# Kernel tuning notes

Hardware: AMD Instinct MI355X
Metric: run time of the kernel (lower is better)

## Reference

```python
import jax, jax.numpy as jnp
import numpy as np


def setup_inputs() -> dict:
    key = jax.random.key(0)
    k1, k2, k3, k4 = jax.random.split(key, 4)
    B, N, D = 4, 2048, 1024
    scale = 1.0 / np.sqrt(D)
    return {
        "x": jax.random.normal(k1, (B, N, D), dtype=jnp.float32),
        "Wq": jax.random.normal(k2, (D, D), dtype=jnp.float32) * scale,
        "Wk": jax.random.normal(k3, (D, D), dtype=jnp.float32) * scale,
        "Wv": jax.random.normal(k4, (D, D), dtype=jnp.float32) * scale,
    }


def reference(x, Wq, Wk, Wv):
    # x: [b, n, d_in]; W*: [d_out, d_in] (torch Linear convention y = x @ W.T)
    q = jnp.einsum("bnd,od->bno", x, Wq)
    k = jnp.einsum("bnd,od->bno", x, Wk)
    v = jnp.einsum("bnd,od->bno", x, Wv)
    n = x.shape[1]
    d_out = k.shape[-1]
    scores = jnp.einsum("bqd,bkd->bqk", q, k)  # [b, n, n]
    causal = jnp.triu(jnp.ones((n, n), dtype=bool), k=1)  # True above diagonal
    scores = jnp.where(causal[None, :, :], -jnp.inf, scores)
    # NOTE: faithful to source -- softmax over dim=1 (query axis), not dim=-1
    attn = jax.nn.softmax(scores / jnp.sqrt(jnp.float32(d_out)), axis=1)
    # dropout p=0.0 (eval): identity
    return jnp.einsum("bqk,bkd->bqd", attn, v)
```

## Files before the change

### kernel.cpp

```cpp
#include <hip/hip_runtime.h>
#include <stdint.h>
#include <math.h>


typedef __attribute__((ext_vector_type(8))) short short8;
typedef __attribute__((ext_vector_type(4))) float f32x4;

static __device__ __forceinline__ ushort f2bf(float f) {
  union { float f; uint32_t u; } v; v.f = f;
  uint32_t r = v.u + 0x7FFFu + ((v.u >> 16) & 1u);
  return (ushort)(r >> 16);
}
static __device__ __forceinline__ float bf2f(ushort u) {
  union { uint32_t u; float f; } v; v.u = ((uint32_t)u) << 16;
  return v.f;
}

static __device__ __forceinline__ void gload_lds16(const ushort* g, ushort* l) {
  __builtin_amdgcn_global_load_lds(
      (const __attribute__((address_space(1))) void*)g,
      (__attribute__((address_space(3))) void*)l, 16, 0, 0);
}

#define SBAR()   __builtin_amdgcn_s_barrier()
#define SCHED0() __builtin_amdgcn_sched_barrier(0)
#define WAITL0() do { asm volatile("s_waitcnt lgkmcnt(0)" ::: "memory"); SCHED0(); } while (0)
#define WAITV4() asm volatile("s_waitcnt vmcnt(4)" ::: "memory")
#define WAITV3() asm volatile("s_waitcnt vmcnt(3)" ::: "memory")
#define WAITV0() asm volatile("s_waitcnt vmcnt(0)" ::: "memory")

__global__ void cast_all(const float* __restrict__ x, const float* __restrict__ Wq,
                         const float* __restrict__ Wk, const float* __restrict__ Wv,
                         ushort* __restrict__ xb, ushort* __restrict__ Wb,
                         int n_x4, int n_w4) {
  int i = blockIdx.x * blockDim.x + threadIdx.x;
  const float* src; ushort* dst; int off;
  if (i < n_x4) { src = x; dst = xb; off = i; }
  else {
    int j = i - n_x4;
    int z = j / n_w4;
    off = j - z * n_w4;
    src = (z == 0) ? Wq : (z == 1) ? Wk : Wv;
    dst = Wb + (long)z * n_w4 * 4;
  }
  float4 v = ((const float4*)src)[off];
  ushort4 o;
  o.x = f2bf(v.x); o.y = f2bf(v.y); o.z = f2bf(v.z); o.w = f2bf(v.w);
  ((ushort4*)dst)[off] = o;
}

__global__ __launch_bounds__(512, 4) void proj_all(
    const ushort* __restrict__ xb, const ushort* __restrict__ Wb,
    ushort* __restrict__ QK, ushort* __restrict__ Vt)
{
  const int D = 1024;
  const long BND = 8388608;
  int L = blockIdx.x;
  L = (L & 7) * 96 + (L >> 3);

  const ushort* Ab; const ushort* Bb;
  int bm0, bn0;
  if (L < 512) {
    int rem = L & 255;
    bm0 = (rem >> 3) * 256;
    bn0 = (rem & 7) * 128;
    Ab = xb;
    Bb = Wb + (long)(L >> 8) * D * D;
  } else {
    int rem = L - 512;
    bm0 = (rem >> 6) * 256;
    bn0 = (rem & 63) * 128;
    Ab = Wb + 2L * D * D;
    Bb = xb;
  }

  const int nk = 32;

  __shared__ uint4 lds_v[73728 / 16];
  char* lds = (char*)lds_v;

  const int tid  = threadIdx.x;
  const int lane = tid & 63;
  const int wave = tid >> 6;
  const int wr   = wave >> 1;
  const int wc   = wave & 1;
  const int fr   = lane & 15;
  const int fg   = lane >> 4;

  f32x4 acc[4][4];
#pragma unroll
  for (int i = 0; i < 4; ++i)
#pragma unroll
    for (int j = 0; j < 4; ++j) acc[i][j] = (f32x4){0.f, 0.f, 0.f, 0.f};

  auto STAGE = [&](int tt) {
    if (tt >= nk) return;
    char* slab = lds + (tt % 3) * 24576;
#pragma unroll
    for (int u = 0; u < 2; ++u) {
      int s = u * 512 + tid;
      int row = s >> 2;
      int cc = (s & 3) ^ ((row >> 1) & 3);
      gload_lds16(Ab + (long)(bm0 + row) * D + tt * 32 + cc * 8,
                  (ushort*)(slab + s * 16));
    }
    {
      int s = tid;
      int row = s >> 2;
      int cc = (s & 3) ^ ((row >> 1) & 3);
      gload_lds16(Bb + (long)(bn0 + row) * D + tt * 32 + cc * 8,
                  (ushort*)(slab + 16384 + s * 16));
    }
  };

  STAGE(0); STAGE(1);
  WAITV3();
  SBAR();

  for (int t = 0; t < nk; ++t) {
    char* slab = lds + (t % 3) * 24576;
    STAGE(t + 2);

    short8 a[4], b[4];
#pragma unroll
    for (int i = 0; i < 4; ++i) {
      int row = wr * 64 + i * 16 + fr;
      int cc = fg ^ ((row >> 1) & 3);
      a[i] = *(const short8*)(slab + row * 64 + cc * 16);
    }
#pragma unroll
    for (int j = 0; j < 4; ++j) {
      int row = wc * 64 + j * 16 + fr;
      int cc = fg ^ ((row >> 1) & 3);
      b[j] = *(const short8*)(slab + 16384 + row * 64 + cc * 16);
    }
    WAITL0();
    __builtin_amdgcn_s_setprio(1);
#pragma unroll
    for (int i = 0; i < 4; ++i)
#pragma unroll
      for (int j = 0; j < 4; ++j)
        acc[i][j] = __builtin_amdgcn_mfma_f32_16x16x32_bf16(a[i], b[j], acc[i][j], 0, 0, 0);
    __builtin_amdgcn_s_setprio(0);

    if (t + 2 < nk) { WAITV3(); } else { WAITV0(); }
    SBAR();
  }

  if (L < 512) {
    ushort* Cb = QK + (long)(L >> 8) * BND;
#pragma unroll
    for (int i = 0; i < 4; ++i)
#pragma unroll
      for (int j = 0; j < 4; ++j)
#pragma unroll
        for (int r = 0; r < 4; ++r) {
          int row = bm0 + wr * 64 + i * 16 + fg * 4 + r;
          int col = bn0 + wc * 64 + j * 16 + fr;
          Cb[(long)row * D + col] = f2bf(acc[i][j][r]);
        }
  } else {
    ushort* Cb = Vt + (long)(bn0 >> 11) * D * 2048;
#pragma unroll
    for (int i = 0; i < 4; ++i)
#pragma unroll
      for (int j = 0; j < 4; ++j)
#pragma unroll
        for (int r = 0; r < 4; ++r) {
          int row = bm0 + wr * 64 + i * 16 + fg * 4 + r;
          int col = (bn0 + wc * 64 + j * 16 + fr) & 2047;
          Cb[(long)row * 2048 + col] = f2bf(acc[i][j][r]);
        }
  }
}

__global__ __launch_bounds__(256, 3) void gemm_s(
    const ushort* __restrict__ Q, const ushort* __restrict__ Kb, ushort* __restrict__ S,
    float* __restrict__ pMg, float* __restrict__ pZg)
{
  const int NQ = 2048, D = 1024;
  int bid = blockIdx.x;
  bid = (bid & 7) * 68 + (bid >> 3);
  const int b = bid / 136;
  int t = bid - b * 136;
  int i = (int)((sqrtf(8.f * t + 1.f) - 1.f) * 0.5f);
  while ((i + 1) * (i + 2) / 2 <= t) ++i;
  while (i * (i + 1) / 2 > t) --i;
  const int j = t - i * (i + 1) / 2;
  const int bm0 = i * 128;
  const int bn0 = j * 128;

  const ushort* Ab = Q + (long)b * NQ * D;
  const ushort* Bb = Kb + (long)b * NQ * D;

  const int nk = 32;

  __shared__ uint4 lds_v[49152 / 16];
  char* lds = (char*)lds_v;

  const int tid  = threadIdx.x;
  const int lane = tid & 63;
  const int wave = tid >> 6;
  const int wr   = wave >> 1;
  const int wc   = wave & 1;
  const int fr   = lane & 15;
  const int fg   = lane >> 4;

  f32x4 acc[4][4];
#pragma unroll
  for (int ii = 0; ii < 4; ++ii)
#pragma unroll
    for (int jj = 0; jj < 4; ++jj) acc[ii][jj] = (f32x4){0.f, 0.f, 0.f, 0.f};

  auto STAGE = [&](int tt) {
    if (tt >= nk) return;
    char* slab = lds + (tt % 3) * 16384;
#pragma unroll
    for (int u = 0; u < 2; ++u) {
      int s = u * 256 + tid;
      int row = s >> 2;
      int cc = (s & 3) ^ ((row >> 1) & 3);
      gload_lds16(Ab + (long)(bm0 + row) * D + tt * 32 + cc * 8,
                  (ushort*)(slab + s * 16));
    }
#pragma unroll
    for (int u = 0; u < 2; ++u) {
      int s = u * 256 + tid;
      int row = s >> 2;
      int cc = (s & 3) ^ ((row >> 1) & 3);
      gload_lds16(Bb + (long)(bn0 + row) * D + tt * 32 + cc * 8,
                  (ushort*)(slab + 8192 + s * 16));
    }
  };

  STAGE(0); STAGE(1);
  WAITV4();
  SBAR();

  for (int tt = 0; tt < nk; ++tt) {
    char* slab = lds + (tt % 3) * 16384;
    STAGE(tt + 2);

    short8 a[4], bf[4];
#pragma unroll
    for (int ii = 0; ii < 4; ++ii) {
      int row = wr * 64 + ii * 16 + fr;
      int cc = fg ^ ((row >> 1) & 3);
      a[ii] = *(const short8*)(slab + row * 64 + cc * 16);
    }
#pragma unroll
    for (int jj = 0; jj < 4; ++jj) {
      int row = wc * 64 + jj * 16 + fr;
      int cc = fg ^ ((row >> 1) & 3);
      bf[jj] = *(const short8*)(slab + 8192 + row * 64 + cc * 16);
    }
    WAITL0();
    __builtin_amdgcn_s_setprio(1);
#pragma unroll
    for (int ii = 0; ii < 4; ++ii)
#pragma unroll
      for (int jj = 0; jj < 4; ++jj)
        acc[ii][jj] = __builtin_amdgcn_mfma_f32_16x16x32_bf16(a[ii], bf[jj], acc[ii][jj], 0, 0, 0);
    __builtin_amdgcn_s_setprio(0);

    if (tt + 2 < nk) { WAITV4(); } else { WAITV0(); }
    SBAR();
  }

  ushort* Cb = S + (long)b * NQ * NQ;
  float mcol[4];
#pragma unroll
  for (int jj = 0; jj < 4; ++jj) {
    const int colg = bn0 + wc * 64 + jj * 16 + fr;
    float m = -3.0e38f;
#pragma unroll
    for (int ii = 0; ii < 4; ++ii)
#pragma unroll
      for (int r = 0; r < 4; ++r) {
        int rowg = bm0 + wr * 64 + ii * 16 + fg * 4 + r;
        float v = acc[ii][jj][r] * 0.03125f;
        acc[ii][jj][r] = v;
        bool ok = rowg >= colg;
        Cb[(long)rowg * NQ + colg] = f2bf(ok ? __expf(v) : 0.f);
        m = ok ? fmaxf(m, v) : m;
      }
    m = fmaxf(m, __shfl_xor(m, 16));
    m = fmaxf(m, __shfl_xor(m, 32));
    mcol[jj] = m;
  }
  float* red = (float*)lds;
  if (fg == 0) {
#pragma unroll
    for (int jj = 0; jj < 4; ++jj)
      red[wr * 128 + wc * 64 + jj * 16 + fr] = mcol[jj];
  }
  SBAR();
  float Mf[4], zcol[4];
#pragma unroll
  for (int jj = 0; jj < 4; ++jj) {
    const int c = wc * 64 + jj * 16 + fr;
    Mf[jj] = fmaxf(red[c], red[128 + c]);
    const int colg = bn0 + c;
    float z = 0.f;
#pragma unroll
    for (int ii = 0; ii < 4; ++ii)
#pragma unroll
      for (int r = 0; r < 4; ++r) {
        int rowg = bm0 + wr * 64 + ii * 16 + fg * 4 + r;
        z += (rowg >= colg) ? __expf(acc[ii][jj][r] - Mf[jj]) : 0.f;
      }
    z += __shfl_xor(z, 16);
    z += __shfl_xor(z, 32);
    zcol[jj] = z;
  }
  if (fg == 0) {
#pragma unroll
    for (int jj = 0; jj < 4; ++jj)
      red[256 + wr * 128 + wc * 64 + jj * 16 + fr] = zcol[jj];
  }
  SBAR();
  if (wr == 0 && fg == 0) {
#pragma unroll
    for (int jj = 0; jj < 4; ++jj) {
      const int c = wc * 64 + jj * 16 + fr;
      long o = ((long)b * 16 + i) * NQ + bn0 + c;
      pMg[o] = Mf[jj];
      pZg[o] = red[256 + c] + red[256 + 128 + c];
    }
  }
}

__global__ void colstats_combine(const float* __restrict__ pM, const float* __restrict__ pZ,
                                 float* __restrict__ cvec, int Nq) {
  int idx = blockIdx.x * 256 + threadIdx.x;
  int b = idx / Nq, k = idx - b * Nq;
  const int i0 = k >> 7;
  const float* PM = pM + (long)b * 16 * Nq + k;
  const float* PZ = pZ + (long)b * 16 * Nq + k;
  float M = -3.0e38f;
  for (int c = i0; c < 16; ++c) M = fmaxf(M, PM[(long)c * Nq]);
  float Z = 0.f;
  for (int c = i0; c < 16; ++c) Z += PZ[(long)c * Nq] * __expf(PM[(long)c * Nq] - M);
  cvec[idx] = __expf(-M) / Z;
}

__global__ void scale_vt(ushort* __restrict__ Vt, const float* __restrict__ cvec,
                         int Nq, int Dd) {
  long t = (long)blockIdx.x * 256 + threadIdx.x;
  long nrow = t / (Nq / 8);
  int nb = (int)(t % (Nq / 8)) * 8;
  int b = (int)(nrow / Dd);
  ushort* p = Vt + nrow * Nq + nb;
  const float* c = cvec + (long)b * Nq + nb;
  union { uint4 v; ushort u[8]; } d, o;
  d.v = *(const uint4*)p;
#pragma unroll
  for (int j = 0; j < 8; ++j) o.u[j] = f2bf(bf2f(d.u[j]) * c[j]);
  *(uint4*)p = o.v;
}

__global__ __launch_bounds__(512, 4) void gemm_pv(
    const ushort* __restrict__ P, const ushort* __restrict__ Vt, float* __restrict__ out)
{
  const int NQ = 2048, DD = 1024;
  int L = blockIdx.x;
  L = (L & 7) * 64 + (L >> 3);
  const int pr = L & 7, dt = (L >> 3) & 15, b = L >> 7;

  const ushort* Pb = P + (long)b * NQ * NQ;
  const ushort* Vb = Vt + (long)b * DD * NQ + (long)(dt * 64) * NQ;
  float* Ob = out + (long)b * NQ * DD;

  __shared__ uint4 lds_v[73728 / 16];
  char* lds = (char*)lds_v;

  const int tid  = threadIdx.x;
  const int lane = tid & 63;
  const int wave = tid >> 6;
  const int wr   = wave >> 1;
  const int wc   = wave & 1;
  const int fr   = lane & 15;
  const int fg   = lane >> 4;

  for (int h = 0; h < 2; ++h) {
    const int tq = h ? (15 - pr) : pr;
    const int q0 = tq * 128;
    const ushort* Aq = Pb + (long)q0 * NQ;
    const int nk = (tq + 1) * 2;

    f32x4 acc[2][2];
#pragma unroll
    for (int i = 0; i < 2; ++i)
#pragma unroll
      for (int j = 0; j < 2; ++j) acc[i][j] = (f32x4){0.f, 0.f, 0.f, 0.f};

    auto STAGE = [&](int tt) {
      if (tt >= nk) return;
      char* slab = lds + (tt % 3) * 24576;
#pragma unroll
      for (int u = 0; u < 2; ++u) {
        int s = u * 512 + tid;
        int row = s >> 3;
        int cc = (s & 7) ^ (row & 7);
        gload_lds16(Aq + (long)row * NQ + tt * 64 + cc * 8,
                    (ushort*)(slab + s * 16));
      }
      {
        int s = tid;
        int row = s >> 3;
        int cc = (s & 7) ^ (row & 7);
        gload_lds16(Vb + (long)row * NQ + tt * 64 + cc * 8,
                    (ushort*)(slab + 16384 + s * 16));
      }
    };

    STAGE(0); STAGE(1);
    WAITV3();
    SBAR();

    for (int t = 0; t < nk; ++t) {
      char* slab = lds + (t % 3) * 24576;
      STAGE(t + 2);

#pragma unroll
      for (int kh = 0; kh < 2; ++kh) {
        short8 a[2], bfr[2];
#pragma unroll
        for (int i = 0; i < 2; ++i) {
          int row = wr * 32 + i * 16 + fr;
          int cc = (kh * 4 + fg) ^ (row & 7);
          a[i] = *(const short8*)(slab + row * 128 + cc * 16);
        }
#pragma unroll
        for (int j = 0; j < 2; ++j) {
          int row = wc * 32 + j * 16 + fr;
          int cc = (kh * 4 + fg) ^ (row & 7);
          bfr[j] = *(const short8*)(slab + 16384 + row * 128 + cc * 16);
        }
        WAITL0();
        __builtin_amdgcn_s_setprio(1);
#pragma unroll
        for (int i = 0; i < 2; ++i)
#pragma unroll
          for (int j = 0; j < 2; ++j)
            acc[i][j] = __builtin_amdgcn_mfma_f32_16x16x32_bf16(a[i], bfr[j], acc[i][j], 0, 0, 0);
        __builtin_amdgcn_s_setprio(0);
      }

      if (t + 2 < nk) { WAITV3(); } else { WAITV0(); }
      SBAR();
    }

#pragma unroll
    for (int i = 0; i < 2; ++i)
#pragma unroll
      for (int j = 0; j < 2; ++j)
#pragma unroll
        for (int r = 0; r < 4; ++r) {
          int row = q0 + wr * 32 + i * 16 + fg * 4 + r;
          int col = dt * 64 + wc * 32 + j * 16 + fr;
          Ob[(long)row * DD + col] = acc[i][j][r];
        }
  }
}

extern "C" void kernel_launch(void* const* d_in, const int* in_sizes, int n_in,
                              void* d_out, int out_size, void* d_ws, size_t ws_size,
                              hipStream_t stream) {
  const float* x  = (const float*)d_in[0];
  const float* Wq = (const float*)d_in[1];
  const float* Wk = (const float*)d_in[2];
  const float* Wv = (const float*)d_in[3];
  float* out = (float*)d_out;

  const int B = 4, N = 2048, D = 1024;
  const long BND = (long)B * N * D;

  char* ws = (char*)d_ws;
  ushort* xb  = (ushort*)ws;
  ushort* Wb  = xb + BND;
  ushort* QK  = Wb + 3L * D * D;
  ushort* Qb  = QK;
  ushort* Kb  = QK + BND;
  ushort* Vt  = QK + 2 * BND;
  ushort* S   = Vt + BND;
  float*  pM  = (float*)(S + (long)B * N * N);
  float*  pZ  = pM + (long)B * 16 * N;
  float*  cv  = pZ + (long)B * 16 * N;

  {
    int n_x4 = (int)(BND / 4);
    int n_w4 = D * D / 4;
    int total = n_x4 + 3 * n_w4;
    cast_all<<<total / 256, 256, 0, stream>>>(x, Wq, Wk, Wv, xb, Wb, n_x4, n_w4);
  }

  proj_all<<<768, 512, 0, stream>>>(xb, Wb, QK, Vt);

  gemm_s<<<544, 256, 0, stream>>>(Qb, Kb, S, pM, pZ);

  colstats_combine<<<(B * N) / 256, 256, 0, stream>>>(pM, pZ, cv, N);

  scale_vt<<<(int)(BND / 8 / 256), 256, 0, stream>>>(Vt, cv, N, D);

  gemm_pv<<<512, 512, 0, stream>>>(S, Vt, out);
}
```

Baseline: 149.8 us.

## Fold Wq and Wk into one matrix G so scores use x·G·xᵀ

Rewrites the scores as q·kᵀ = x·(Wqᵀ·Wk)·xᵀ. A small GEMM now precomputes G = Wqᵀ·Wk, then a single projection H = x·G replaces the separate Q and K projections, and the score GEMM reads H and x directly. This removes one of the three large projection GEMMs and the K write and read, at the cost of an extra D×D GEMM, a transposing cast kernel, and rounding G to bf16, which adds numerical error.

```diff
diff --git a/kernel.cpp b/kernel.cpp
--- a/kernel.cpp
+++ b/kernel.cpp
@@ -29,54 +29,48 @@
 #define WAITV3() asm volatile("s_waitcnt vmcnt(3)" ::: "memory")
 #define WAITV0() asm volatile("s_waitcnt vmcnt(0)" ::: "memory")
 
-__global__ void cast_all(const float* __restrict__ x, const float* __restrict__ Wq,
-                         const float* __restrict__ Wk, const float* __restrict__ Wv,
-                         ushort* __restrict__ xb, ushort* __restrict__ Wb,
+__global__ void cast_all(const float* __restrict__ x, const float* __restrict__ Wv,
+                         ushort* __restrict__ xb, ushort* __restrict__ Wvb,
                          int n_x4, int n_w4) {
   int i = blockIdx.x * blockDim.x + threadIdx.x;
   const float* src; ushort* dst; int off;
   if (i < n_x4) { src = x; dst = xb; off = i; }
-  else {
-    int j = i - n_x4;
-    int z = j / n_w4;
-    off = j - z * n_w4;
-    src = (z == 0) ? Wq : (z == 1) ? Wk : Wv;
-    dst = Wb + (long)z * n_w4 * 4;
-  }
+  else { src = Wv; dst = Wvb; off = i - n_x4; }
   float4 v = ((const float4*)src)[off];
   ushort4 o;
   o.x = f2bf(v.x); o.y = f2bf(v.y); o.z = f2bf(v.z); o.w = f2bf(v.w);
   ((ushort4*)dst)[off] = o;
 }
 
-__global__ __launch_bounds__(512, 4) void proj_all(
-    const ushort* __restrict__ xb, const ushort* __restrict__ Wb,
-    ushort* __restrict__ QK, ushort* __restrict__ Vt)
+__global__ void cast_w_t(const float* __restrict__ Wq, const float* __restrict__ Wk,
+                         ushort* __restrict__ WqT, ushort* __restrict__ WkT) {
+  __shared__ ushort t[64][65];
+  const float* src = blockIdx.z ? Wk : Wq;
+  ushort* dst = blockIdx.z ? WkT : WqT;
+  int c0 = blockIdx.x * 64, r0 = blockIdx.y * 64;
+  int tid = threadIdx.x;
+#pragma unroll
+  for (int i = 0; i < 16; ++i) {
+    int idx = i * 256 + tid, r = idx >> 6, c = idx & 63;
+    t[r][c] = f2bf(src[(long)(r0 + r) * 1024 + c0 + c]);
+  }
+  __syncthreads();
+#pragma unroll
+  for (int i = 0; i < 16; ++i) {
+    int idx = i * 256 + tid, r = idx >> 6, c = idx & 63;
+    dst[(long)(c0 + r) * 1024 + r0 + c] = t[c][r];
+  }
+}
+
+__global__ __launch_bounds__(256, 3) void gemm_g(
+    const ushort* __restrict__ WkT, const ushort* __restrict__ WqT, ushort* __restrict__ Gt)
 {
   const int D = 1024;
-  const long BND = 8388608;
-  int L = blockIdx.x;
-  L = (L & 7) * 96 + (L >> 3);
-
-  const ushort* Ab; const ushort* Bb;
-  int bm0, bn0;
-  if (L < 512) {
-    int rem = L & 255;
-    bm0 = (rem >> 3) * 256;
-    bn0 = (rem & 7) * 128;
-    Ab = xb;
-    Bb = Wb + (long)(L >> 8) * D * D;
-  } else {
-    int rem = L - 512;
-    bm0 = (rem >> 6) * 256;
-    bn0 = (rem & 63) * 128;
-    Ab = Wb + 2L * D * D;
-    Bb = xb;
-  }
-
+  const int bm0 = blockIdx.x * 128;
+  const int bn0 = blockIdx.y * 128;
   const int nk = 32;
 
-  __shared__ uint4 lds_v[73728 / 16];
+  __shared__ uint4 lds_v[49152 / 16];
   char* lds = (char*)lds_v;
 
   const int tid  = threadIdx.x;
@@ -89,6 +83,111 @@
 
   f32x4 acc[4][4];
 #pragma unroll
+  for (int ii = 0; ii < 4; ++ii)
+#pragma unroll
+    for (int jj = 0; jj < 4; ++jj) acc[ii][jj] = (f32x4){0.f, 0.f, 0.f, 0.f};
+
+  auto STAGE = [&](int tt) {
+    if (tt >= nk) return;
+    char* slab = lds + (tt % 3) * 16384;
+#pragma unroll
+    for (int u = 0; u < 2; ++u) {
+      int s = u * 256 + tid;
+      int row = s >> 2;
+      int cc = (s & 3) ^ ((row >> 1) & 3);
+      gload_lds16(WkT + (long)(bm0 + row) * D + tt * 32 + cc * 8,
+                  (ushort*)(slab + s * 16));
+    }
+#pragma unroll
+    for (int u = 0; u < 2; ++u) {
+      int s = u * 256 + tid;
+      int row = s >> 2;
+      int cc = (s & 3) ^ ((row >> 1) & 3);
+      gload_lds16(WqT + (long)(bn0 + row) * D + tt * 32 + cc * 8,
+                  (ushort*)(slab + 8192 + s * 16));
+    }
+  };
+
+  STAGE(0); STAGE(1);
+  WAITV4();
+  SBAR();
+
+  for (int tt = 0; tt < nk; ++tt) {
+    char* slab = lds + (tt % 3) * 16384;
+    STAGE(tt + 2);
+    short8 a[4], bf[4];
+#pragma unroll
+    for (int ii = 0; ii < 4; ++ii) {
+      int row = wr * 64 + ii * 16 + fr;
+      int cc = fg ^ ((row >> 1) & 3);
+      a[ii] = *(const short8*)(slab + row * 64 + cc * 16);
+    }
+#pragma unroll
+    for (int jj = 0; jj < 4; ++jj) {
+      int row = wc * 64 + jj * 16 + fr;
+      int cc = fg ^ ((row >> 1) & 3);
+      bf[jj] = *(const short8*)(slab + 8192 + row * 64 + cc * 16);
+    }
+    WAITL0();
+    __builtin_amdgcn_s_setprio(1);
+#pragma unroll
+    for (int ii = 0; ii < 4; ++ii)
+#pragma unroll
+      for (int jj = 0; jj < 4; ++jj)
+        acc[ii][jj] = __builtin_amdgcn_mfma_f32_16x16x32_bf16(a[ii], bf[jj], acc[ii][jj], 0, 0, 0);
+    __builtin_amdgcn_s_setprio(0);
+    if (tt + 2 < nk) { WAITV4(); } else { WAITV0(); }
+    SBAR();
+  }
+
+#pragma unroll
+  for (int ii = 0; ii < 4; ++ii)
+#pragma unroll
+    for (int jj = 0; jj < 4; ++jj)
+#pragma unroll
+      for (int r = 0; r < 4; ++r) {
+        int row = bm0 + wr * 64 + ii * 16 + fg * 4 + r;
+        int col = bn0 + wc * 64 + jj * 16 + fr;
+        Gt[(long)row * D + col] = f2bf(acc[ii][jj][r]);
+      }
+}
+
+__global__ __launch_bounds__(512, 4) void proj_all(
+    const ushort* __restrict__ xb, const ushort* __restrict__ Gt,
+    const ushort* __restrict__ Wv, ushort* __restrict__ H, ushort* __restrict__ Vt)
+{
+  const int D = 1024;
+  int L = blockIdx.x;
+  L = (L & 7) * 64 + (L >> 3);
+
+  const ushort* Ab; const ushort* Bb;
+  int bm0, bn0;
+  if (L < 256) {
+    bm0 = (L >> 3) * 256;
+    bn0 = (L & 7) * 128;
+    Ab = xb;  Bb = Gt;
+  } else {
+    int rem = L - 256;
+    bm0 = (rem >> 6) * 256;
+    bn0 = (rem & 63) * 128;
+    Ab = Wv;  Bb = xb;
+  }
+
+  const int nk = 32;
+
+  __shared__ uint4 lds_v[73728 / 16];
+  char* lds = (char*)lds_v;
+
+  const int tid  = threadIdx.x;
+  const int lane = tid & 63;
+  const int wave = tid >> 6;
+  const int wr   = wave >> 1;
+  const int wc   = wave & 1;
+  const int fr   = lane & 15;
+  const int fg   = lane >> 4;
+
+  f32x4 acc[4][4];
+#pragma unroll
   for (int i = 0; i < 4; ++i)
 #pragma unroll
     for (int j = 0; j < 4; ++j) acc[i][j] = (f32x4){0.f, 0.f, 0.f, 0.f};
@@ -147,8 +246,8 @@
     SBAR();
   }
 
-  if (L < 512) {
-    ushort* Cb = QK + (long)(L >> 8) * BND;
+  if (L < 256) {
+    ushort* Cb = H;
 #pragma unroll
     for (int i = 0; i < 4; ++i)
 #pragma unroll
@@ -478,11 +577,12 @@
 
   char* ws = (char*)d_ws;
   ushort* xb  = (ushort*)ws;
-  ushort* Wb  = xb + BND;
-  ushort* QK  = Wb + 3L * D * D;
-  ushort* Qb  = QK;
-  ushort* Kb  = QK + BND;
-  ushort* Vt  = QK + 2 * BND;
+  ushort* WqT = xb + BND;
+  ushort* WkT = WqT + (long)D * D;
+  ushort* Wvb = WkT + (long)D * D;
+  ushort* Gt  = Wvb + (long)D * D;
+  ushort* Hb  = Gt + (long)D * D;
+  ushort* Vt  = Hb + BND;
   ushort* S   = Vt + BND;
   float*  pM  = (float*)(S + (long)B * N * N);
   float*  pZ  = pM + (long)B * 16 * N;
@@ -491,13 +591,21 @@
   {
     int n_x4 = (int)(BND / 4);
     int n_w4 = D * D / 4;
-    int total = n_x4 + 3 * n_w4;
-    cast_all<<<total / 256, 256, 0, stream>>>(x, Wq, Wk, Wv, xb, Wb, n_x4, n_w4);
-  }
-
-  proj_all<<<768, 512, 0, stream>>>(xb, Wb, QK, Vt);
-
-  gemm_s<<<544, 256, 0, stream>>>(Qb, Kb, S, pM, pZ);
+    cast_all<<<(n_x4 + n_w4) / 256, 256, 0, stream>>>(x, Wv, xb, Wvb, n_x4, n_w4);
+  }
+  {
+    dim3 g(16, 16, 2);
+    cast_w_t<<<g, 256, 0, stream>>>(Wq, Wk, WqT, WkT);
+  }
+
+  {
+    dim3 g(8, 8);
+    gemm_g<<<g, 256, 0, stream>>>(WkT, WqT, Gt);
+  }
+
+  proj_all<<<512, 512, 0, stream>>>(xb, Gt, Wvb, Hb, Vt);
+
+  gemm_s<<<544, 256, 0, stream>>>(Hb, xb, S, pM, pZ);
 
   colstats_combine<<<(B * N) / 256, 256, 0, stream>>>(pM, pZ, cv, N);
 
```

New measurement: 149.5 us. No clear change (-0.2%).
